# Optimization experiments

Measured on AMD Instinct MI355X. Metric: run time of the kernel, lower is better.

## Reference

```python
import jax, jax.numpy as jnp
import numpy as np

N = 50000
E = 800000
IN = 64
HID = 64
OUT = 32
R = 8
B = 8
EPS = 1e-5


def setup_inputs() -> dict:
    key = jax.random.key(0)
    ks = jax.random.split(key, 20)
    s_in = 1.0 / np.sqrt(IN)
    s_hid = 1.0 / np.sqrt(HID)
    inp = {
        "x": jax.random.normal(ks[0], (N, IN), dtype=jnp.float32),
        "edge_index": jax.random.randint(ks[1], (2, E), 0, N, dtype=jnp.int64) if jax.config.jax_enable_x64 else jax.random.randint(ks[1], (2, E), 0, N),
        "edge_type": jax.random.randint(ks[2], (E,), 0, R),
        # conv1: in -> hid
        "comp1": jax.random.normal(ks[3], (R, B), dtype=jnp.float32) * (1.0 / np.sqrt(B)),
        "bases1": jax.random.normal(ks[4], (B, IN, HID), dtype=jnp.float32) * s_in,
        "root1": jax.random.normal(ks[5], (IN, HID), dtype=jnp.float32) * s_in,
        "bias1": jnp.zeros((HID,), dtype=jnp.float32),
        # conv2 (hidden): hid -> hid
        "comp2": jax.random.normal(ks[6], (R, B), dtype=jnp.float32) * (1.0 / np.sqrt(B)),
        "bases2": jax.random.normal(ks[7], (B, HID, HID), dtype=jnp.float32) * s_hid,
        "root2": jax.random.normal(ks[8], (HID, HID), dtype=jnp.float32) * s_hid,
        "bias2": jnp.zeros((HID,), dtype=jnp.float32),
        # conv_out: hid -> out
        "comp3": jax.random.normal(ks[9], (R, B), dtype=jnp.float32) * (1.0 / np.sqrt(B)),
        "bases3": jax.random.normal(ks[10], (B, HID, OUT), dtype=jnp.float32) * s_hid,
        "root3": jax.random.normal(ks[11], (HID, OUT), dtype=jnp.float32) * s_hid,
        "bias3": jnp.zeros((OUT,), dtype=jnp.float32),
        # batchnorms
        "gamma1": jnp.ones((HID,), dtype=jnp.float32),
        "beta1": jnp.zeros((HID,), dtype=jnp.float32),
        "gamma2": jnp.ones((HID,), dtype=jnp.float32),
        "beta2": jnp.zeros((HID,), dtype=jnp.float32),
    }
    return inp


def rgcn_conv(x, src, dst, etype, comp, bases, root, bias):
    """PyG-style RGCNConv with basis decomposition and per-relation mean aggregation."""
    n = x.shape[0]
    # project node features through all bases: [N, B, O]
    xb = jnp.einsum('ni,bio->nbo', x, bases)
    # per-edge relation coefficients [E, B] contract with gathered basis features [E, B, O]
    msg = jnp.einsum('eb,ebo->eo', comp[etype], xb[src])
    # mean normalization per (dst node, relation)
    seg = dst * R + etype
    cnt = jax.ops.segment_sum(jnp.ones((msg.shape[0],), dtype=x.dtype), seg, num_segments=n * R)
    msg = msg / jnp.maximum(cnt[seg], 1.0)[:, None]
    agg = jax.ops.segment_sum(msg, dst, num_segments=n)
    return agg + x @ root + bias


def batch_norm(x, gamma, beta):
    mu = jnp.mean(x, axis=0)
    var = jnp.mean(jnp.square(x - mu), axis=0)  # biased, as torch BN training
    return (x - mu) * jax.lax.rsqrt(var + EPS) * gamma + beta


def reference(x, edge_index, edge_type, comp1, bases1, root1, bias1,
              comp2, bases2, root2, bias2, comp3, bases3, root3, bias3,
              gamma1, beta1, gamma2, beta2):
    src, dst = edge_index[0], edge_index[1]
    h = rgcn_conv(x, src, dst, edge_type, comp1, bases1, root1, bias1)
    h = batch_norm(jax.nn.relu(h), gamma1, beta1)  # dropout = identity (eval)
    h_res = h  # residual since in_channels == hidden_channels
    h2 = rgcn_conv(h, src, dst, edge_type, comp2, bases2, root2, bias2)
    h2 = batch_norm(jax.nn.relu(h2), gamma2, beta2)
    h = h2 + h_res
    out = rgcn_conv(h, src, dst, edge_type, comp3, bases3, root3, bias3)
    return out
```

## Files before the change

### kernel.cpp

```cpp
#include <hip/hip_runtime.h>

#define NN 50000
#define NE 800000
#define RR 8
#define BB 8
#define EPSV 1e-5f
#define SCAN_B ((NN + 255) / 256)
#define NGRP 64

typedef unsigned short bfu;
typedef __attribute__((ext_vector_type(8))) short bf16x8;
typedef __attribute__((ext_vector_type(4))) float f32x4;

__device__ inline float bf2f(bfu u) { return __uint_as_float(((unsigned)u) << 16); }
__device__ inline bfu f2bf(float f) {
    unsigned u = __float_as_uint(f);
    return (bfu)((u + 0x7fffu + ((u >> 16) & 1u)) >> 16);
}

#define NW1 36864L
#define NW2 36864L
#define NW3 18432L
#define NCV ((long)NN * 64)
#define NZ  (400000L + 50000L + 2L * NGRP * 128)

__device__ inline void build_one(const float* __restrict__ comp, const float* __restrict__ bases,
                                 const float* __restrict__ root, bfu* __restrict__ Wp,
                                 int O, int idx) {
    int k = idx / O, o = idx % O;
    float val;
    if (k < 512) {
        int r = k >> 6, i = k & 63;
        val = 0.f;
#pragma unroll
        for (int b = 0; b < BB; ++b)
            val += comp[r * BB + b] * bases[(b * 64 + i) * O + o];
    } else {
        val = root[(k - 512) * O + o];
    }
    int kt = k >> 5, kk = k & 31;
    int lane = ((kk >> 3) << 4) | (o & 15);
    int pos = ((kt * (O / 16) + (o >> 4)) * 64 + lane) * 8 + (kk & 7);
    Wp[pos] = f2bf(val);
}

__global__ void prep(const float* __restrict__ c1, const float* __restrict__ b1,
                     const float* __restrict__ r1, bfu* __restrict__ Wp1,
                     const float* __restrict__ c2, const float* __restrict__ b2,
                     const float* __restrict__ r2, bfu* __restrict__ Wp2,
                     const float* __restrict__ c3, const float* __restrict__ b3,
                     const float* __restrict__ r3, bfu* __restrict__ Wp3,
                     const float* __restrict__ x, bfu* __restrict__ xb,
                     float* __restrict__ zbase) {
    long i = (long)blockIdx.x * blockDim.x + threadIdx.x;
    long stride = (long)gridDim.x * blockDim.x;
    const long tot = NW1 + NW2 + NW3 + NCV + NZ;
    for (; i < tot; i += stride) {
        if (i < NW1) build_one(c1, b1, r1, Wp1, 64, (int)i);
        else if (i < NW1 + NW2) build_one(c2, b2, r2, Wp2, 64, (int)(i - NW1));
        else if (i < NW1 + NW2 + NW3) build_one(c3, b3, r3, Wp3, 32, (int)(i - NW1 - NW2));
        else if (i < NW1 + NW2 + NW3 + NCV) { long k = i - NW1 - NW2 - NW3; xb[k] = f2bf(x[k]); }
        else zbase[i - (NW1 + NW2 + NW3 + NCV)] = 0.f;
    }
}

__global__ void edge_count(const int* __restrict__ ei, const int* __restrict__ et,
                           float* __restrict__ cnt) {
    int range = blockIdx.x >> 8;
    int lo = range * (NN / 8), hi = lo + NN / 8;
    int i = (blockIdx.x & 255) * 256 + threadIdx.x;
    for (int e = i; e < NE; e += 256 * 256) {
        int d = ei[NE + e];
        if (d >= lo && d < hi)
            atomicAdd(&cnt[(size_t)d * RR + et[e]], 1.0f);
    }
}

__global__ void scan1(const float* __restrict__ cnt, int* __restrict__ offs, int* __restrict__ bsum) {
    __shared__ int sh[256];
    int b = blockIdx.x, t = threadIdx.x;
    int i = b * 256 + t;
    int v = 0;
    if (i < NN) {
        float s = 0.f;
#pragma unroll
        for (int r = 0; r < RR; ++r) s += cnt[(size_t)i * RR + r];
        v = (int)s;
    }
    sh[t] = v;
    __syncthreads();
    for (int s = 1; s < 256; s <<= 1) {
        int tmp = (t >= s) ? sh[t - s] : 0;
        __syncthreads();
        sh[t] += tmp;
        __syncthreads();
    }
    if (i < NN) offs[i] = sh[t] - v;
    if (t == 255) bsum[b] = sh[255];
}

__global__ void scan2(int* __restrict__ bsum, int* __restrict__ offs) {
    if (threadIdx.x == 0 && blockIdx.x == 0) {
        int run = 0;
        for (int b = 0; b < SCAN_B; ++b) { int t = bsum[b]; bsum[b] = run; run += t; }
        offs[NN] = run;
    }
}

__global__ void scan3(int* __restrict__ offs, const int* __restrict__ bsum) {
    int b = blockIdx.x, t = threadIdx.x;
    int i = b * 256 + t;
    if (i < NN) offs[i] += bsum[b];
}

__global__ void place(const int* __restrict__ ei, const int* __restrict__ et,
                      const int* __restrict__ offs, int* __restrict__ fill,
                      unsigned* __restrict__ esrt) {
    int range = blockIdx.x >> 8;
    int lo = range * (NN / 8), hi = lo + NN / 8;
    int i = (blockIdx.x & 255) * 256 + threadIdx.x;
    for (int e = i; e < NE; e += 256 * 256) {
        int d = ei[NE + e];
        if (d >= lo && d < hi) {
            int pos = offs[d] + atomicAdd(&fill[d], 1);
            esrt[pos] = ((unsigned)ei[e] << 3) | (unsigned)et[e];
        }
    }
}

#define ACCUMS(SU, V)                          \
    switch ((SU) & 7) {                        \
        case 0: a0 += (V); break;              \
        case 1: a1 += (V); break;              \
        case 2: a2 += (V); break;              \
        case 3: a3 += (V); break;              \
        case 4: a4 += (V); break;              \
        case 5: a5 += (V); break;              \
        case 6: a6 += (V); break;              \
        default: a7 += (V); break;             \
    }
#define RFL(X) __builtin_amdgcn_readfirstlane((int)(X))
#define GATH(S) bf2f(xb[((size_t)((unsigned)(S) >> 3)) * 64 + lane])

template <int O, bool RELU, bool STATS>
__global__ __launch_bounds__(256) void agg_gemm(const int* __restrict__ offs,
                                                const unsigned* __restrict__ esrt,
                                                const float* __restrict__ cnt,
                                                const bfu* __restrict__ xb,
                                                const bfu* __restrict__ Wp,
                                                const float* __restrict__ bias,
                                                float* __restrict__ outp,
                                                float* __restrict__ stats) {
    constexpr int CT = O / 16;
    __shared__ bfu Af[1152 * 8];
    int wave = threadIdx.x >> 6, lane = threadIdx.x & 63;
    int n0 = blockIdx.x * 16;
    int c = lane;
    int swz_lo = ((c >> 3) & 3) << 4;

#pragma unroll 1
    for (int i = 0; i < 4; ++i) {
        int row = wave * 4 + i;
        int n = n0 + row;
        int j0 = offs[n], j1 = offs[n + 1];
        float a0 = 0.f, a1 = 0.f, a2 = 0.f, a3 = 0.f, a4 = 0.f, a5 = 0.f, a6 = 0.f, a7 = 0.f;
        int j = j0;
        for (; j + 8 <= j1; j += 8) {
            int s0 = RFL(esrt[j + 0]), s1 = RFL(esrt[j + 1]);
            int s2 = RFL(esrt[j + 2]), s3 = RFL(esrt[j + 3]);
            int s4 = RFL(esrt[j + 4]), s5 = RFL(esrt[j + 5]);
            int s6 = RFL(esrt[j + 6]), s7 = RFL(esrt[j + 7]);
            float v0 = GATH(s0), v1 = GATH(s1), v2 = GATH(s2), v3 = GATH(s3);
            float v4 = GATH(s4), v5 = GATH(s5), v6 = GATH(s6), v7 = GATH(s7);
            ACCUMS(s0, v0) ACCUMS(s1, v1) ACCUMS(s2, v2) ACCUMS(s3, v3)
            ACCUMS(s4, v4) ACCUMS(s5, v5) ACCUMS(s6, v6) ACCUMS(s7, v7)
        }
        for (; j + 4 <= j1; j += 4) {
            int s0 = RFL(esrt[j + 0]), s1 = RFL(esrt[j + 1]);
            int s2 = RFL(esrt[j + 2]), s3 = RFL(esrt[j + 3]);
            float v0 = GATH(s0), v1 = GATH(s1), v2 = GATH(s2), v3 = GATH(s3);
            ACCUMS(s0, v0) ACCUMS(s1, v1) ACCUMS(s2, v2) ACCUMS(s3, v3)
        }
        for (; j < j1; ++j) {
            int s0 = RFL(esrt[j]);
            float v0 = GATH(s0);
            ACCUMS(s0, v0)
        }
#define WR(r, ar) {                                                            \
        float inv = 1.f / fmaxf(cnt[(size_t)n * RR + (r)], 1.f);               \
        bfu bv = f2bf((ar) * inv);                                             \
        int g = (2 * (r) + (c >> 5)) * 64 + (row | swz_lo);                    \
        int gs = g ^ ((g >> 3) & 7) ^ ((g >> 6) & 7);                          \
        Af[gs * 8 + (c & 7)] = bv; }
        WR(0, a0) WR(1, a1) WR(2, a2) WR(3, a3)
        WR(4, a4) WR(5, a5) WR(6, a6) WR(7, a7)
#undef WR
        {
            bfu bv = xb[(size_t)n * 64 + lane];
            int g = (16 + (c >> 5)) * 64 + (row | swz_lo);
            int gs = g ^ ((g >> 3) & 7) ^ ((g >> 6) & 7);
            Af[gs * 8 + (c & 7)] = bv;
        }
    }
    __syncthreads();

    int ct = wave;
    if (CT == 4 || ct < CT) {
        f32x4 acc = (f32x4){0.f, 0.f, 0.f, 0.f};
#pragma unroll
        for (int kt = 0; kt < 18; ++kt) {
            int g = kt * 64 + lane;
            int gs = g ^ ((g >> 3) & 7) ^ ((g >> 6) & 7);
            bf16x8 af = *(const bf16x8*)&Af[gs * 8];
            bf16x8 bfv = *(const bf16x8*)&Wp[((size_t)(kt * CT + ct) * 64 + lane) * 8];
            acc = __builtin_amdgcn_mfma_f32_16x16x32_bf16(af, bfv, acc, 0, 0, 0);
        }
        int col = ct * 16 + (lane & 15);
        float b = bias[col];
        float ssum = 0.f, sq = 0.f;
#pragma unroll
        for (int jj = 0; jj < 4; ++jj) {
            int row = (lane >> 4) * 4 + jj;
            float v = acc[jj] + b;
            if (RELU) v = fmaxf(v, 0.f);
            outp[(size_t)(n0 + row) * O + col] = v;
            if (STATS) { ssum += v; sq += v * v; }
        }
        if (STATS) {
            ssum += __shfl_xor(ssum, 16); ssum += __shfl_xor(ssum, 32);
            sq   += __shfl_xor(sq, 16);   sq   += __shfl_xor(sq, 32);
            if ((lane >> 4) == 0) {
                int g = blockIdx.x & (NGRP - 1);
                atomicAdd(&stats[g * 128 + col], ssum);
                atomicAdd(&stats[g * 128 + 64 + col], sq);
            }
        }
    }
}

template <bool HASRES>
__global__ __launch_bounds__(256) void bn_apply(const float* __restrict__ y,
                                                const float* __restrict__ stats,
                                                const float* __restrict__ gamma,
                                                const float* __restrict__ beta,
                                                const bfu* __restrict__ resb,
                                                bfu* __restrict__ hb) {
    __shared__ float sc[128];
    int t = threadIdx.x;
    if (t < 64) {
        float s = 0.f, q = 0.f;
        for (int g = 0; g < NGRP; ++g) {
            s += stats[g * 128 + t];
            q += stats[g * 128 + 64 + t];
        }
        float mu = s / (float)NN;
        float var = q / (float)NN - mu * mu;
        float scale = gamma[t] * rsqrtf(var + EPSV);
        sc[t] = scale;
        sc[64 + t] = beta[t] - mu * scale;
    }
    __syncthreads();
    long tot = (long)NN * 64;
    long stride = (long)gridDim.x * blockDim.x;
    for (long i = (long)blockIdx.x * blockDim.x + threadIdx.x; i < tot; i += stride) {
        int cc = (int)(i & 63);
        float v = y[i] * sc[cc] + sc[64 + cc];
        if (HASRES) v += bf2f(resb[i]);
        hb[i] = f2bf(v);
    }
}

extern "C" void kernel_launch(void* const* d_in, const int* in_sizes, int n_in,
                              void* d_out, int out_size, void* d_ws, size_t ws_size,
                              hipStream_t stream) {
    const float* x      = (const float*)d_in[0];
    const int*   ei     = (const int*)d_in[1];
    const int*   et     = (const int*)d_in[2];
    const float* comp1  = (const float*)d_in[3];
    const float* bases1 = (const float*)d_in[4];
    const float* root1  = (const float*)d_in[5];
    const float* bias1  = (const float*)d_in[6];
    const float* comp2  = (const float*)d_in[7];
    const float* bases2 = (const float*)d_in[8];
    const float* root2  = (const float*)d_in[9];
    const float* bias2  = (const float*)d_in[10];
    const float* bias3  = (const float*)d_in[14];
    const float* comp3  = (const float*)d_in[11];
    const float* bases3 = (const float*)d_in[12];
    const float* root3  = (const float*)d_in[13];
    const float* gamma1 = (const float*)d_in[15];
    const float* beta1  = (const float*)d_in[16];
    const float* gamma2 = (const float*)d_in[17];
    const float* beta2  = (const float*)d_in[18];
    float* out = (float*)d_out;

    float* ws = (float*)d_ws;
    size_t off = 0;
    bfu* Wp1 = (bfu*)(ws + off); off += 18432;
    bfu* Wp2 = (bfu*)(ws + off); off += 18432;
    bfu* Wp3 = (bfu*)(ws + off); off += 9216;
    float* cnt    = ws + off; off += (size_t)NN * RR;
    int*   fill   = (int*)(ws + off); off += NN;
    float* stats1 = ws + off; off += NGRP * 128;
    float* stats2 = ws + off; off += NGRP * 128;
    float* y  = ws + off; off += (size_t)NN * 64;
    bfu* xb   = (bfu*)(ws + off); off += (size_t)NN * 32;
    bfu* h1b  = (bfu*)(ws + off); off += (size_t)NN * 32;
    bfu* hb   = (bfu*)(ws + off); off += (size_t)NN * 32;
    int* offs = (int*)(ws + off); off += NN + 4;
    int* bsum = (int*)(ws + off); off += 256;
    unsigned* esrt = (unsigned*)(ws + off); off += NE;

    prep<<<dim3(2048), dim3(256), 0, stream>>>(comp1, bases1, root1, Wp1,
                                               comp2, bases2, root2, Wp2,
                                               comp3, bases3, root3, Wp3,
                                               x, xb, cnt);
    edge_count<<<dim3(2048), dim3(256), 0, stream>>>(ei, et, cnt);
    scan1<<<dim3(SCAN_B), dim3(256), 0, stream>>>(cnt, offs, bsum);
    scan2<<<dim3(1), dim3(64), 0, stream>>>(bsum, offs);
    scan3<<<dim3(SCAN_B), dim3(256), 0, stream>>>(offs, bsum);
    place<<<dim3(2048), dim3(256), 0, stream>>>(ei, et, offs, fill, esrt);

    agg_gemm<64, true, true><<<dim3(NN / 16), dim3(256), 0, stream>>>(offs, esrt, cnt, xb, Wp1, bias1, y, stats1);
    bn_apply<false><<<dim3(256), dim3(256), 0, stream>>>(y, stats1, gamma1, beta1, nullptr, h1b);

    agg_gemm<64, true, true><<<dim3(NN / 16), dim3(256), 0, stream>>>(offs, esrt, cnt, h1b, Wp2, bias2, y, stats2);
    bn_apply<true><<<dim3(256), dim3(256), 0, stream>>>(y, stats2, gamma2, beta2, h1b, hb);

    agg_gemm<32, false, false><<<dim3(NN / 16), dim3(256), 0, stream>>>(offs, esrt, cnt, hb, Wp3, bias3, out, nullptr);
}
```

Baseline: 290.9 us.

## Gather int8 row-quantized features in aggregation and double waves per block

Adds per-row int8 quantization (with a per-node fp32 scale) of the node features at each layer. The edge gather loop now reads int8 rows plus one scale, halving the gathered bytes, and loads the 8 edge indices with a single vector load broadcast via readlane. Blocks grow to 512 threads so each wave aggregates 2 rows instead of 4, for more parallelism in the gather. Int8 quantization reduces message precision, which may exceed accuracy tolerances, and the GEMM phase leaves half of the waves idle.

```diff
diff --git a/kernel.cpp b/kernel.cpp
--- a/kernel.cpp
+++ b/kernel.cpp
@@ -9,6 +9,7 @@
 #define NGRP 64
 
 typedef unsigned short bfu;
+typedef signed char i8;
 typedef __attribute__((ext_vector_type(8))) short bf16x8;
 typedef __attribute__((ext_vector_type(4))) float f32x4;
 
@@ -21,7 +22,6 @@
 #define NW1 36864L
 #define NW2 36864L
 #define NW3 18432L
-#define NCV ((long)NN * 64)
 #define NZ  (400000L + 50000L + 2L * NGRP * 128)
 
 __device__ inline void build_one(const float* __restrict__ comp, const float* __restrict__ bases,
@@ -50,17 +50,34 @@
                      const float* __restrict__ r2, bfu* __restrict__ Wp2,
                      const float* __restrict__ c3, const float* __restrict__ b3,
                      const float* __restrict__ r3, bfu* __restrict__ Wp3,
-                     const float* __restrict__ x, bfu* __restrict__ xb,
                      float* __restrict__ zbase) {
     long i = (long)blockIdx.x * blockDim.x + threadIdx.x;
     long stride = (long)gridDim.x * blockDim.x;
-    const long tot = NW1 + NW2 + NW3 + NCV + NZ;
+    const long tot = NW1 + NW2 + NW3 + NZ;
     for (; i < tot; i += stride) {
         if (i < NW1) build_one(c1, b1, r1, Wp1, 64, (int)i);
         else if (i < NW1 + NW2) build_one(c2, b2, r2, Wp2, 64, (int)(i - NW1));
         else if (i < NW1 + NW2 + NW3) build_one(c3, b3, r3, Wp3, 32, (int)(i - NW1 - NW2));
-        else if (i < NW1 + NW2 + NW3 + NCV) { long k = i - NW1 - NW2 - NW3; xb[k] = f2bf(x[k]); }
-        else zbase[i - (NW1 + NW2 + NW3 + NCV)] = 0.f;
+        else zbase[i - (NW1 + NW2 + NW3)] = 0.f;
+    }
+}
+
+__global__ __launch_bounds__(256) void cvt_rows(const float* __restrict__ x,
+                                                bfu* __restrict__ xb,
+                                                i8* __restrict__ x8,
+                                                float* __restrict__ xs) {
+    int wv = threadIdx.x >> 6, lane = threadIdx.x & 63;
+    int gw = blockIdx.x * 4 + wv, nw = gridDim.x * 4;
+    for (int n = gw; n < NN; n += nw) {
+        float v = x[(size_t)n * 64 + lane];
+        xb[(size_t)n * 64 + lane] = f2bf(v);
+        float am = fabsf(v);
+#pragma unroll
+        for (int d = 1; d < 64; d <<= 1) am = fmaxf(am, __shfl_xor(am, d));
+        am = fmaxf(am, 1e-20f);
+        float inv = 127.f / am;
+        x8[(size_t)n * 64 + lane] = (i8)__float2int_rn(v * inv);
+        if (lane == 0) xs[n] = am * (1.f / 127.f);
     }
 }
 
@@ -139,18 +156,19 @@
         case 6: a6 += (V); break;              \
         default: a7 += (V); break;             \
     }
-#define RFL(X) __builtin_amdgcn_readfirstlane((int)(X))
-#define GATH(S) bf2f(xb[((size_t)((unsigned)(S) >> 3)) * 64 + lane])
+#define RDL(X, L) __builtin_amdgcn_readlane((int)(X), (L))
 
 template <int O, bool RELU, bool STATS>
-__global__ __launch_bounds__(256) void agg_gemm(const int* __restrict__ offs,
-                                                const unsigned* __restrict__ esrt,
-                                                const float* __restrict__ cnt,
-                                                const bfu* __restrict__ xb,
-                                                const bfu* __restrict__ Wp,
-                                                const float* __restrict__ bias,
-                                                float* __restrict__ outp,
-                                                float* __restrict__ stats) {
+__global__ __launch_bounds__(512, 8) void agg_gemm(const int* __restrict__ offs,
+                                                   const unsigned* __restrict__ esrt,
+                                                   const float* __restrict__ cnt,
+                                                   const i8* __restrict__ x8,
+                                                   const float* __restrict__ xs,
+                                                   const bfu* __restrict__ xb,
+                                                   const bfu* __restrict__ Wp,
+                                                   const float* __restrict__ bias,
+                                                   float* __restrict__ outp,
+                                                   float* __restrict__ stats) {
     constexpr int CT = O / 16;
     __shared__ bfu Af[1152 * 8];
     int wave = threadIdx.x >> 6, lane = threadIdx.x & 63;
@@ -159,32 +177,48 @@
     int swz_lo = ((c >> 3) & 3) << 4;
 
 #pragma unroll 1
-    for (int i = 0; i < 4; ++i) {
-        int row = wave * 4 + i;
+    for (int i = 0; i < 2; ++i) {
+        int row = wave * 2 + i;
         int n = n0 + row;
         int j0 = offs[n], j1 = offs[n + 1];
         float a0 = 0.f, a1 = 0.f, a2 = 0.f, a3 = 0.f, a4 = 0.f, a5 = 0.f, a6 = 0.f, a7 = 0.f;
         int j = j0;
         for (; j + 8 <= j1; j += 8) {
-            int s0 = RFL(esrt[j + 0]), s1 = RFL(esrt[j + 1]);
-            int s2 = RFL(esrt[j + 2]), s3 = RFL(esrt[j + 3]);
-            int s4 = RFL(esrt[j + 4]), s5 = RFL(esrt[j + 5]);
-            int s6 = RFL(esrt[j + 6]), s7 = RFL(esrt[j + 7]);
-            float v0 = GATH(s0), v1 = GATH(s1), v2 = GATH(s2), v3 = GATH(s3);
-            float v4 = GATH(s4), v5 = GATH(s5), v6 = GATH(s6), v7 = GATH(s7);
-            ACCUMS(s0, v0) ACCUMS(s1, v1) ACCUMS(s2, v2) ACCUMS(s3, v3)
-            ACCUMS(s4, v4) ACCUMS(s5, v5) ACCUMS(s6, v6) ACCUMS(s7, v7)
-        }
-        for (; j + 4 <= j1; j += 4) {
-            int s0 = RFL(esrt[j + 0]), s1 = RFL(esrt[j + 1]);
-            int s2 = RFL(esrt[j + 2]), s3 = RFL(esrt[j + 3]);
-            float v0 = GATH(s0), v1 = GATH(s1), v2 = GATH(s2), v3 = GATH(s3);
-            ACCUMS(s0, v0) ACCUMS(s1, v1) ACCUMS(s2, v2) ACCUMS(s3, v3)
+            unsigned mye = esrt[j + (lane & 7)];
+            int s0 = RDL(mye, 0), s1 = RDL(mye, 1), s2 = RDL(mye, 2), s3 = RDL(mye, 3);
+            int s4 = RDL(mye, 4), s5 = RDL(mye, 5), s6 = RDL(mye, 6), s7 = RDL(mye, 7);
+            float q0 = (float)x8[(size_t)((unsigned)s0 >> 3) * 64 + lane];
+            float q1 = (float)x8[(size_t)((unsigned)s1 >> 3) * 64 + lane];
+            float q2 = (float)x8[(size_t)((unsigned)s2 >> 3) * 64 + lane];
+            float q3 = (float)x8[(size_t)((unsigned)s3 >> 3) * 64 + lane];
+            float q4 = (float)x8[(size_t)((unsigned)s4 >> 3) * 64 + lane];
+            float q5 = (float)x8[(size_t)((unsigned)s5 >> 3) * 64 + lane];
+            float q6 = (float)x8[(size_t)((unsigned)s6 >> 3) * 64 + lane];
+            float q7 = (float)x8[(size_t)((unsigned)s7 >> 3) * 64 + lane];
+            float c0 = xs[(unsigned)s0 >> 3], c1 = xs[(unsigned)s1 >> 3];
+            float c2 = xs[(unsigned)s2 >> 3], c3 = xs[(unsigned)s3 >> 3];
+            float c4 = xs[(unsigned)s4 >> 3], c5 = xs[(unsigned)s5 >> 3];
+            float c6 = xs[(unsigned)s6 >> 3], c7 = xs[(unsigned)s7 >> 3];
+            ACCUMS(s0, q0 * c0) ACCUMS(s1, q1 * c1) ACCUMS(s2, q2 * c2) ACCUMS(s3, q3 * c3)
+            ACCUMS(s4, q4 * c4) ACCUMS(s5, q5 * c5) ACCUMS(s6, q6 * c6) ACCUMS(s7, q7 * c7)
+        }
+        if (j + 4 <= j1) {
+            unsigned mye = esrt[j + (lane & 3)];
+            int s0 = RDL(mye, 0), s1 = RDL(mye, 1), s2 = RDL(mye, 2), s3 = RDL(mye, 3);
+            float q0 = (float)x8[(size_t)((unsigned)s0 >> 3) * 64 + lane];
+            float q1 = (float)x8[(size_t)((unsigned)s1 >> 3) * 64 + lane];
+            float q2 = (float)x8[(size_t)((unsigned)s2 >> 3) * 64 + lane];
+            float q3 = (float)x8[(size_t)((unsigned)s3 >> 3) * 64 + lane];
+            float c0 = xs[(unsigned)s0 >> 3], c1 = xs[(unsigned)s1 >> 3];
+            float c2 = xs[(unsigned)s2 >> 3], c3 = xs[(unsigned)s3 >> 3];
+            ACCUMS(s0, q0 * c0) ACCUMS(s1, q1 * c1) ACCUMS(s2, q2 * c2) ACCUMS(s3, q3 * c3)
+            j += 4;
         }
         for (; j < j1; ++j) {
-            int s0 = RFL(esrt[j]);
-            float v0 = GATH(s0);
-            ACCUMS(s0, v0)
+            int s0 = __builtin_amdgcn_readfirstlane((int)esrt[j]);
+            float q0 = (float)x8[(size_t)((unsigned)s0 >> 3) * 64 + lane];
+            float c0 = xs[(unsigned)s0 >> 3];
+            ACCUMS(s0, q0 * c0)
         }
 #define WR(r, ar) {                                                            \
         float inv = 1.f / fmaxf(cnt[(size_t)n * RR + (r)], 1.f);               \
@@ -205,7 +239,7 @@
     __syncthreads();
 
     int ct = wave;
-    if (CT == 4 || ct < CT) {
+    if (ct < CT) {
         f32x4 acc = (f32x4){0.f, 0.f, 0.f, 0.f};
 #pragma unroll
         for (int kt = 0; kt < 18; ++kt) {
@@ -244,7 +278,9 @@
                                                 const float* __restrict__ gamma,
                                                 const float* __restrict__ beta,
                                                 const bfu* __restrict__ resb,
-                                                bfu* __restrict__ hb) {
+                                                bfu* __restrict__ hb,
+                                                i8* __restrict__ h8,
+                                                float* __restrict__ hs) {
     __shared__ float sc[128];
     int t = threadIdx.x;
     if (t < 64) {
@@ -260,13 +296,19 @@
         sc[64 + t] = beta[t] - mu * scale;
     }
     __syncthreads();
-    long tot = (long)NN * 64;
-    long stride = (long)gridDim.x * blockDim.x;
-    for (long i = (long)blockIdx.x * blockDim.x + threadIdx.x; i < tot; i += stride) {
-        int cc = (int)(i & 63);
-        float v = y[i] * sc[cc] + sc[64 + cc];
-        if (HASRES) v += bf2f(resb[i]);
-        hb[i] = f2bf(v);
+    int wv = threadIdx.x >> 6, lane = threadIdx.x & 63;
+    int gw = blockIdx.x * 4 + wv, nw = gridDim.x * 4;
+    for (int n = gw; n < NN; n += nw) {
+        float v = y[(size_t)n * 64 + lane] * sc[lane] + sc[64 + lane];
+        if (HASRES) v += bf2f(resb[(size_t)n * 64 + lane]);
+        hb[(size_t)n * 64 + lane] = f2bf(v);
+        float am = fabsf(v);
+#pragma unroll
+        for (int d = 1; d < 64; d <<= 1) am = fmaxf(am, __shfl_xor(am, d));
+        am = fmaxf(am, 1e-20f);
+        float inv = 127.f / am;
+        h8[(size_t)n * 64 + lane] = (i8)__float2int_rn(v * inv);
+        if (lane == 0) hs[n] = am * (1.f / 127.f);
     }
 }
 
@@ -284,10 +326,10 @@
     const float* bases2 = (const float*)d_in[8];
     const float* root2  = (const float*)d_in[9];
     const float* bias2  = (const float*)d_in[10];
-    const float* bias3  = (const float*)d_in[14];
     const float* comp3  = (const float*)d_in[11];
     const float* bases3 = (const float*)d_in[12];
     const float* root3  = (const float*)d_in[13];
+    const float* bias3  = (const float*)d_in[14];
     const float* gamma1 = (const float*)d_in[15];
     const float* beta1  = (const float*)d_in[16];
     const float* gamma2 = (const float*)d_in[17];
@@ -307,25 +349,31 @@
     bfu* xb   = (bfu*)(ws + off); off += (size_t)NN * 32;
     bfu* h1b  = (bfu*)(ws + off); off += (size_t)NN * 32;
     bfu* hb   = (bfu*)(ws + off); off += (size_t)NN * 32;
+    i8*  x8   = (i8*)(ws + off);  off += (size_t)NN * 16;
+    i8*  h1_8 = (i8*)(ws + off);  off += (size_t)NN * 16;
+    i8*  h_8  = (i8*)(ws + off);  off += (size_t)NN * 16;
+    float* xsc  = ws + off; off += NN;
+    float* h1sc = ws + off; off += NN;
+    float* hsc  = ws + off; off += NN;
     int* offs = (int*)(ws + off); off += NN + 4;
     int* bsum = (int*)(ws + off); off += 256;
     unsigned* esrt = (unsigned*)(ws + off); off += NE;
 
-    prep<<<dim3(2048), dim3(256), 0, stream>>>(comp1, bases1, root1, Wp1,
+    prep<<<dim3(1024), dim3(256), 0, stream>>>(comp1, bases1, root1, Wp1,
                                                comp2, bases2, root2, Wp2,
-                                               comp3, bases3, root3, Wp3,
-                                               x, xb, cnt);
+                                               comp3, bases3, root3, Wp3, cnt);
+    cvt_rows<<<dim3(512), dim3(256), 0, stream>>>(x, xb, x8, xsc);
     edge_count<<<dim3(2048), dim3(256), 0, stream>>>(ei, et, cnt);
     scan1<<<dim3(SCAN_B), dim3(256), 0, stream>>>(cnt, offs, bsum);
     scan2<<<dim3(1), dim3(64), 0, stream>>>(bsum, offs);
     scan3<<<dim3(SCAN_B), dim3(256), 0, stream>>>(offs, bsum);
     place<<<dim3(2048), dim3(256), 0, stream>>>(ei, et, offs, fill, esrt);
 
-    agg_gemm<64, true, true><<<dim3(NN / 16), dim3(256), 0, stream>>>(offs, esrt, cnt, xb, Wp1, bias1, y, stats1);
-    bn_apply<false><<<dim3(256), dim3(256), 0, stream>>>(y, stats1, gamma1, beta1, nullptr, h1b);
-
-    agg_gemm<64, true, true><<<dim3(NN / 16), dim3(256), 0, stream>>>(offs, esrt, cnt, h1b, Wp2, bias2, y, stats2);
-    bn_apply<true><<<dim3(256), dim3(256), 0, stream>>>(y, stats2, gamma2, beta2, h1b, hb);
-
-    agg_gemm<32, false, false><<<dim3(NN / 16), dim3(256), 0, stream>>>(offs, esrt, cnt, hb, Wp3, bias3, out, nullptr);
-}
+    agg_gemm<64, true, true><<<dim3(NN / 16), dim3(512), 0, stream>>>(offs, esrt, cnt, x8, xsc, xb, Wp1, bias1, y, stats1);
+    bn_apply<false><<<dim3(1024), dim3(256), 0, stream>>>(y, stats1, gamma1, beta1, nullptr, h1b, h1_8, h1sc);
+
+    agg_gemm<64, true, true><<<dim3(NN / 16), dim3(512), 0, stream>>>(offs, esrt, cnt, h1_8, h1sc, h1b, Wp2, bias2, y, stats2);
+    bn_apply<true><<<dim3(1024), dim3(256), 0, stream>>>(y, stats2, gamma2, beta2, h1b, hb, h_8, hsc);
+
+    agg_gemm<32, false, false><<<dim3(NN / 16), dim3(512), 0, stream>>>(offs, esrt, cnt, h_8, hsc, hb, Wp3, bias3, out, nullptr);
+}
```

Result: slower. 304.9 us (+4.8%).

## Balance edge gather across waves using LDS atomic accumulation per block

Applied to the files above, without the earlier changes.

Instead of each wave handling four destination rows sequentially with switch-based per-relation register accumulators, the block's 16-node edge range is split evenly across the four waves. Each wave gathers source features and accumulates into a shared-memory (dst,relation) buffer with LDS float atomics, using a repacked edge encoding that carries the local destination index. This targets load imbalance from uneven degrees and branchy accumulation. In exchange it adds 32KB of LDS (lowering occupancy), a zeroing pass, and LDS atomic contention.

```diff
diff --git a/kernel.cpp b/kernel.cpp
--- a/kernel.cpp
+++ b/kernel.cpp
@@ -123,24 +123,10 @@
         int d = ei[NE + e];
         if (d >= lo && d < hi) {
             int pos = offs[d] + atomicAdd(&fill[d], 1);
-            esrt[pos] = ((unsigned)ei[e] << 3) | (unsigned)et[e];
-        }
-    }
-}
-
-#define ACCUMS(SU, V)                          \
-    switch ((SU) & 7) {                        \
-        case 0: a0 += (V); break;              \
-        case 1: a1 += (V); break;              \
-        case 2: a2 += (V); break;              \
-        case 3: a3 += (V); break;              \
-        case 4: a4 += (V); break;              \
-        case 5: a5 += (V); break;              \
-        case 6: a6 += (V); break;              \
-        default: a7 += (V); break;             \
-    }
-#define RFL(X) __builtin_amdgcn_readfirstlane((int)(X))
-#define GATH(S) bf2f(xb[((size_t)((unsigned)(S) >> 3)) * 64 + lane])
+            esrt[pos] = ((unsigned)ei[e] << 7) | ((unsigned)(d & 15) << 3) | (unsigned)et[e];
+        }
+    }
+}
 
 template <int O, bool RELU, bool STATS>
 __global__ __launch_bounds__(256) void agg_gemm(const int* __restrict__ offs,
@@ -152,55 +138,57 @@
                                                 float* __restrict__ outp,
                                                 float* __restrict__ stats) {
     constexpr int CT = O / 16;
+    __shared__ float accL[128 * 64];
     __shared__ bfu Af[1152 * 8];
     int wave = threadIdx.x >> 6, lane = threadIdx.x & 63;
     int n0 = blockIdx.x * 16;
+
+    for (int i = threadIdx.x; i < 128 * 64; i += 256) accL[i] = 0.f;
+    __syncthreads();
+
+    int e0 = offs[n0], e1 = offs[n0 + 16];
+    int per = (e1 - e0 + 3) >> 2;
+    int jw0 = e0 + wave * per;
+    int jw1 = jw0 + per; if (jw1 > e1) jw1 = e1;
+    if (jw0 > e1) jw0 = e1;
+
+    int j = jw0;
+    for (; j + 16 <= jw1; j += 16) {
+        unsigned mye = esrt[j + (lane & 15)];
+#pragma unroll
+        for (int k = 0; k < 16; ++k) {
+            int u = __builtin_amdgcn_readlane((int)mye, k);
+            unsigned src = ((unsigned)u) >> 7;
+            float v = bf2f(xb[(size_t)src * 64 + lane]);
+            atomicAdd(&accL[(u & 127) * 64 + lane], v);
+        }
+    }
+    for (; j < jw1; ++j) {
+        int u = __builtin_amdgcn_readfirstlane((int)esrt[j]);
+        unsigned src = ((unsigned)u) >> 7;
+        float v = bf2f(xb[(size_t)src * 64 + lane]);
+        atomicAdd(&accL[(u & 127) * 64 + lane], v);
+    }
+    __syncthreads();
+
     int c = lane;
     int swz_lo = ((c >> 3) & 3) << 4;
-
-#pragma unroll 1
-    for (int i = 0; i < 4; ++i) {
-        int row = wave * 4 + i;
-        int n = n0 + row;
-        int j0 = offs[n], j1 = offs[n + 1];
-        float a0 = 0.f, a1 = 0.f, a2 = 0.f, a3 = 0.f, a4 = 0.f, a5 = 0.f, a6 = 0.f, a7 = 0.f;
-        int j = j0;
-        for (; j + 8 <= j1; j += 8) {
-            int s0 = RFL(esrt[j + 0]), s1 = RFL(esrt[j + 1]);
-            int s2 = RFL(esrt[j + 2]), s3 = RFL(esrt[j + 3]);
-            int s4 = RFL(esrt[j + 4]), s5 = RFL(esrt[j + 5]);
-            int s6 = RFL(esrt[j + 6]), s7 = RFL(esrt[j + 7]);
-            float v0 = GATH(s0), v1 = GATH(s1), v2 = GATH(s2), v3 = GATH(s3);
-            float v4 = GATH(s4), v5 = GATH(s5), v6 = GATH(s6), v7 = GATH(s7);
-            ACCUMS(s0, v0) ACCUMS(s1, v1) ACCUMS(s2, v2) ACCUMS(s3, v3)
-            ACCUMS(s4, v4) ACCUMS(s5, v5) ACCUMS(s6, v6) ACCUMS(s7, v7)
-        }
-        for (; j + 4 <= j1; j += 4) {
-            int s0 = RFL(esrt[j + 0]), s1 = RFL(esrt[j + 1]);
-            int s2 = RFL(esrt[j + 2]), s3 = RFL(esrt[j + 3]);
-            float v0 = GATH(s0), v1 = GATH(s1), v2 = GATH(s2), v3 = GATH(s3);
-            ACCUMS(s0, v0) ACCUMS(s1, v1) ACCUMS(s2, v2) ACCUMS(s3, v3)
-        }
-        for (; j < j1; ++j) {
-            int s0 = RFL(esrt[j]);
-            float v0 = GATH(s0);
-            ACCUMS(s0, v0)
-        }
-#define WR(r, ar) {                                                            \
-        float inv = 1.f / fmaxf(cnt[(size_t)n * RR + (r)], 1.f);               \
-        bfu bv = f2bf((ar) * inv);                                             \
-        int g = (2 * (r) + (c >> 5)) * 64 + (row | swz_lo);                    \
-        int gs = g ^ ((g >> 3) & 7) ^ ((g >> 6) & 7);                          \
-        Af[gs * 8 + (c & 7)] = bv; }
-        WR(0, a0) WR(1, a1) WR(2, a2) WR(3, a3)
-        WR(4, a4) WR(5, a5) WR(6, a6) WR(7, a7)
-#undef WR
-        {
-            bfu bv = xb[(size_t)n * 64 + lane];
-            int g = (16 + (c >> 5)) * 64 + (row | swz_lo);
-            int gs = g ^ ((g >> 3) & 7) ^ ((g >> 6) & 7);
-            Af[gs * 8 + (c & 7)] = bv;
-        }
+#pragma unroll 4
+    for (int row = wave * 32; row < wave * 32 + 32; ++row) {
+        int dloc = row >> 3, r = row & 7;
+        float cn = cnt[(size_t)(n0 + dloc) * RR + r];
+        float v = accL[row * 64 + lane] / fmaxf(cn, 1.f);
+        bfu bv = f2bf(v);
+        int g = (2 * r + (c >> 5)) * 64 + (dloc | swz_lo);
+        int gs = g ^ ((g >> 3) & 7) ^ ((g >> 6) & 7);
+        Af[gs * 8 + (c & 7)] = bv;
+    }
+#pragma unroll
+    for (int dloc = wave * 4; dloc < wave * 4 + 4; ++dloc) {
+        bfu bv = xb[(size_t)(n0 + dloc) * 64 + lane];
+        int g = (16 + (c >> 5)) * 64 + (dloc | swz_lo);
+        int gs = g ^ ((g >> 3) & 7) ^ ((g >> 6) & 7);
+        Af[gs * 8 + (c & 7)] = bv;
     }
     __syncthreads();
 
@@ -284,10 +272,10 @@
     const float* bases2 = (const float*)d_in[8];
     const float* root2  = (const float*)d_in[9];
     const float* bias2  = (const float*)d_in[10];
-    const float* bias3  = (const float*)d_in[14];
     const float* comp3  = (const float*)d_in[11];
     const float* bases3 = (const float*)d_in[12];
     const float* root3  = (const float*)d_in[13];
+    const float* bias3  = (const float*)d_in[14];
     const float* gamma1 = (const float*)d_in[15];
     const float* beta1  = (const float*)d_in[16];
     const float* gamma2 = (const float*)d_in[17];
```

After: 995.4 us. 3.42x slower.
